# Optimization experiments

Measured on AMD Instinct MI355X. Metric: run time of the kernel, lower is better.

## Reference

```python
import jax, jax.numpy as jnp
import numpy as np

STRIDES = (2, 2, 2)  # from init_kwargs


def _sparse_conv3d_transpose(images, kernel, default_value, base_plane, strides):
    """Sparse masked 3D transposed conv driven by a per-pixel depth base plane.

    images:     [B, Hi, Wi, Di, C]  stored slab of active voxels per pixel
    kernel:     [kH, kW, kD, F, C]
    base_plane: [B, Ho, Wo, 1] int  starting VIRTUAL depth of the output slab
    Output virtual depth of voxel (ho, wo, do) is base_plane[ho, wo] + do.
    Input slab start (in input-depth units) at input pixel (hi, wi) is
    base_plane[hi*sH, wi*sW] // sD. SAME-style padding ((k-1)//2).
    Out-of-slab / out-of-bounds taps read default_value (frozen zero).
    """
    B, Hi, Wi, Di, C = images.shape
    k0, k1, k2, F, _ = kernel.shape
    s0, s1, s2 = strides
    bp = base_plane[..., 0]                       # [B, Ho, Wo]
    Ho, Wo = bp.shape[1], bp.shape[2]
    Do = Di * s2
    p0, p1, p2 = (k0 - 1) // 2, (k1 - 1) // 2, (k2 - 1) // 2
    bp_in = bp[:, ::s0, ::s1] // s2               # [B, Hi, Wi] input slab start
    b_idx = jnp.arange(B)[:, None, None]
    vd = bp[..., None] + jnp.arange(Do)           # [B, Ho, Wo, Do] virtual out depth
    ho = jnp.arange(Ho)
    wo = jnp.arange(Wo)
    out = jnp.zeros((B, Ho, Wo, Do, F), images.dtype)
    for kh in range(k0):
        hn = ho + p0 - kh
        hok = (hn % s0 == 0) & (hn >= 0) & (hn < Hi * s0)
        hi = jnp.clip(hn // s0, 0, Hi - 1)
        for kw in range(k1):
            wn = wo + p1 - kw
            wok = (wn % s1 == 0) & (wn >= 0) & (wn < Wi * s1)
            wi = jnp.clip(wn // s1, 0, Wi - 1)
            sp_ok = hok[None, :, None] & wok[None, None, :]              # [1,Ho,Wo]
            bpg = bp_in[b_idx, hi[None, :, None], wi[None, None, :]]     # [B,Ho,Wo]
            for kd in range(k2):
                dn = vd + p2 - kd                                        # [B,Ho,Wo,Do]
                dok = (dn % s2) == 0
                di = dn // s2 - bpg[..., None]
                mask = sp_ok[..., None] & dok & (di >= 0) & (di < Di)
                dic = jnp.clip(di, 0, Di - 1)
                # gather [B,Ho,Wo,Do,C]
                vals = images[b_idx[..., None], hi[None, :, None, None],
                              wi[None, None, :, None], dic]
                vals = jnp.where(mask[..., None], vals, default_value)
                out = out + jnp.einsum('bhwdc,fc->bhwdf', vals, kernel[kh, kw, kd])
    return out


def setup_inputs() -> dict:
    key = jax.random.key(0)
    k1, k2, k3 = jax.random.split(key, 3)
    B, Hi, Wi, Di, C, F = 2, 64, 64, 32, 16, 8
    images = jax.random.normal(k1, (B, Hi, Wi, Di, C), dtype=jnp.float32)
    base_plane = jax.random.randint(k2, (B, Hi * 2, Wi * 2, 1), 0, 16, dtype=jnp.int32)
    kernel = jax.random.normal(k3, (3, 3, 3, F, C), dtype=jnp.float32) * 0.1
    default_value = jnp.zeros((), dtype=jnp.float32)  # frozen, zeros initializer
    return {"images": images, "base_plane": base_plane,
            "kernel": kernel, "default_value": default_value}


def reference(images, base_plane, kernel, default_value):
    return _sparse_conv3d_transpose(images, kernel, default_value, base_plane, STRIDES)
```

## Files before the change

kernel.cpp:

```cpp
#include <hip/hip_runtime.h>

constexpr int Bc  = 2;
constexpr int HiC = 64, WiC = 64, DiC = 32;
constexpr int Cc  = 16, Fc  = 8;
constexpr int HoC = 128, WoC = 128, DoC = 64;

constexpr int SLAB_SHORTS = DiC * Cc;
constexpr int NSLAB       = 18;
constexpr int ZOFF        = NSLAB * SLAB_SHORTS * 2;

typedef __attribute__((ext_vector_type(8))) short short8;
typedef __attribute__((ext_vector_type(4))) float f32x4;

__device__ alignas(16) const float FZERO[8] = {0, 0, 0, 0, 0, 0, 0, 0};

__device__ __forceinline__ unsigned pk2(float x, float y) {
    unsigned ux = __float_as_uint(x), uy = __float_as_uint(y);
    ux += ((ux >> 16) & 1u) + 0x7FFFu;
    uy += ((uy >> 16) & 1u) + 0x7FFFu;
    return (ux >> 16) | (uy & 0xFFFF0000u);
}
__device__ __forceinline__ short8 pack8(float4 a, float4 b) {
    union { unsigned u[4]; short8 s; } r;
    r.u[0] = pk2(a.x, a.y); r.u[1] = pk2(a.z, a.w);
    r.u[2] = pk2(b.x, b.y); r.u[3] = pk2(b.z, b.w);
    return r.s;
}

template<int CLS>
__device__ __forceinline__ void doCols(const short* __restrict__ slabs,
                                       const int*   __restrict__ bp,
                                       const float* __restrict__ kern,
                                       float*       __restrict__ out,
                                       float*       __restrict__ ldsw,
                                       int b, int ho, int wo0, int wi0, int lane) {
    constexpr int NP = (CLS == 0) ? 1 : ((CLS == 3) ? 4 : 2);
    constexpr int OP = (NP + 1) / 2;
    constexpr int KH[4][4] = {{1,0,0,0},{1,1,0,0},{0,2,0,0},{0,0,2,2}};
    constexpr int KW[4][4] = {{1,0,0,0},{0,2,0,0},{1,1,0,0},{0,2,0,2}};

    const int quad = lane >> 4, n = lane & 15;
    const int half = quad >> 1, chalf = quad & 1;
    const int chalfB = chalf * 16;

    short8 bE[NP], bO[OP];
    #pragma unroll
    for (int p = 0; p < NP; ++p) {
        const int kp = KH[CLS][p] * 3 + KW[CLS][p];
        const float* wp = (n < Fc)
            ? kern + (kp * 3 + 2 * half) * 128 + n * 16 + chalf * 8 : FZERO;
        bE[p] = pack8(*(const float4*)wp, *(const float4*)(wp + 4));
    }
    #pragma unroll
    for (int pp = 0; pp < OP; ++pp) {
        const int  PA   = (2 * pp < NP) ? 2 * pp : 0;
        const bool hasB = (2 * pp + 1) < NP;
        const int  PB   = hasB ? (2 * pp + 1) : 0;
        const int kpa = KH[CLS][PA] * 3 + KW[CLS][PA];
        const int kpb = KH[CLS][PB] * 3 + KW[CLS][PB];
        const int kp  = half ? kpb : kpa;
        const bool v  = (n < Fc) && (!half || hasB);
        const float* wp = v ? kern + (kp * 3 + 1) * 128 + n * 16 + chalf * 8 : FZERO;
        bO[pp] = pack8(*(const float4*)wp, *(const float4*)(wp + 4));
    }

    int colx[4], bpcol[4], bpgr[4][NP], pxo[4][NP]; bool pvs[4][NP];
    #pragma unroll
    for (int cc = 0; cc < 4; ++cc) {
        const int wo = wo0 + 2 * cc;
        colx[cc]  = __builtin_amdgcn_readfirstlane((b * HoC + ho) * WoC + wo);
        bpcol[cc] = bp[colx[cc]];
        #pragma unroll
        for (int p = 0; p < NP; ++p) {
            const int kh = KH[CLS][p], kw = KW[CLS][p];
            int hi = (ho + 1 - kh) >> 1; hi = hi > HiC - 1 ? HiC - 1 : hi;
            int wi = (wo + 1 - kw) >> 1; wi = wi > WiC - 1 ? WiC - 1 : wi;
            pvs[cc][p] = (kh != 0 || ho + 1 < HoC) && (kw != 0 || wo + 1 < WoC);
            const int sidx =
                __builtin_amdgcn_readfirstlane((b * HoC + 2 * hi) * WoC + 2 * wi);
            bpgr[cc][p] = bp[sidx];
            const int hidx = (kh == 0) ? 1 : 0;
            pxo[cc][p] = __builtin_amdgcn_readfirstlane(
                             (hidx * 9 + (wi - wi0)) << 10);
        }
    }

    #pragma unroll
    for (int cc = 0; cc < 4; ++cc) {
        const int bp_col = bpcol[cc];
        const int q      = (bp_col + 1) & 1;
        const int baseE  = (bp_col + q + 1) >> 1;
        const int baseO  = (bp_col + 1 - q) >> 1;
        int sE[NP], sO[NP];
        #pragma unroll
        for (int p = 0; p < NP; ++p) {
            const int bpg = bpgr[cc][p] >> 1;
            sE[p] = pvs[cc][p] ? baseE - bpg : -100000;
            sO[p] = pvs[cc][p] ? baseO - bpg : -100000;
        }

        f32x4 accE[2] = {{0.f,0.f,0.f,0.f},{0.f,0.f,0.f,0.f}};
        f32x4 accO[2] = {{0.f,0.f,0.f,0.f},{0.f,0.f,0.f,0.f}};

        #pragma unroll
        for (int g = 0; g < 2; ++g) {
            #pragma unroll
            for (int p = 0; p < NP; ++p) {
                const int  di = sE[p] + 16 * g + n - half;
                const bool ok = (unsigned)di < (unsigned)DiC;
                const int  off = ok ? pxo[cc][p] + di * 32 + chalfB : ZOFF;
                short8 a = *(const short8*)((const char*)slabs + off);
                accE[g] = __builtin_amdgcn_mfma_f32_16x16x32_bf16(a, bE[p], accE[g], 0, 0, 0);
            }
            #pragma unroll
            for (int pp = 0; pp < OP; ++pp) {
                const int  PA   = (2 * pp < NP) ? 2 * pp : 0;
                const bool hasB = (2 * pp + 1) < NP;
                const int  PB   = hasB ? (2 * pp + 1) : 0;
                const int  sOs  = half ? (hasB ? sO[PB] : -100000) : sO[PA];
                const int  pxs  = half ? pxo[cc][PB] : pxo[cc][PA];
                const int  di = sOs + 16 * g + n;
                const bool ok = (unsigned)di < (unsigned)DiC;
                const int  off = ok ? pxs + di * 32 + chalfB : ZOFF;
                short8 a = *(const short8*)((const char*)slabs + off);
                accO[g] = __builtin_amdgcn_mfma_f32_16x16x32_bf16(a, bO[pp], accO[g], 0, 0, 0);
            }
        }

        __builtin_amdgcn_wave_barrier();
        if (n < Fc) {
            #pragma unroll
            for (int g = 0; g < 2; ++g) {
                #pragma unroll
                for (int r = 0; r < 4; ++r) {
                    const int m2 = 16 * g + quad * 4 + r;
                    ldsw[(2 * m2 + q) * Fc + n]     = accE[g][r];
                    ldsw[(2 * m2 + 1 - q) * Fc + n] = accO[g][r];
                }
            }
        }
        __builtin_amdgcn_wave_barrier();
        float* outc = out + (size_t)colx[cc] * (DoC * Fc);
        *(float4*)(outc + lane * 8)     = *(const float4*)(ldsw + lane * 8);
        *(float4*)(outc + lane * 8 + 4) = *(const float4*)(ldsw + lane * 8 + 4);
        __builtin_amdgcn_wave_barrier();
    }
}

__global__ __launch_bounds__(256, 4)
void sconv_mfma(const float* __restrict__ img, const int* __restrict__ bp,
                const float* __restrict__ kern, float* __restrict__ out) {
    __shared__ short slabs[NSLAB * SLAB_SHORTS + 8];
    __shared__ float lds[4 * DoC * Fc];
    const int t = threadIdx.x, wv = t >> 6, lane = t & 63;
    const int b = blockIdx.z, r = blockIdx.y;
    const int wo0 = (blockIdx.x << 4) + (wv & 1) + ((wv >> 1) << 3);
    const int wi0 = blockIdx.x << 3;
    float* ldsw = lds + wv * (DoC * Fc);

    const int hi0 = r;
    int hi1 = r + 1; if (hi1 > HiC - 1) hi1 = HiC - 1;
    #pragma unroll
    for (int k = 0; k < 5; ++k) {
        const int s = wv + 4 * k;
        if (s < NSLAB) {
            const int hi = (s >= 9) ? hi1 : hi0;
            int wi = wi0 + ((s >= 9) ? s - 9 : s); if (wi > WiC - 1) wi = WiC - 1;
            const float* g = img + (((b * HiC + hi) * WiC + wi) << 9) + lane * 8;
            float4 v0 = *(const float4*)g;
            float4 v1 = *(const float4*)(g + 4);
            *(short8*)&slabs[(s << 9) + lane * 8] = pack8(v0, v1);
        }
    }
    if (t < 8) slabs[NSLAB * SLAB_SHORTS + t] = 0;
    __syncthreads();

    if (wv & 1) {
        doCols<1>(slabs, bp, kern, out, ldsw, b, 2 * r,     wo0, wi0, lane);
        doCols<3>(slabs, bp, kern, out, ldsw, b, 2 * r + 1, wo0, wi0, lane);
    } else {
        doCols<0>(slabs, bp, kern, out, ldsw, b, 2 * r,     wo0, wi0, lane);
        doCols<2>(slabs, bp, kern, out, ldsw, b, 2 * r + 1, wo0, wi0, lane);
    }
}

extern "C" void kernel_launch(void* const* d_in, const int* in_sizes, int n_in,
                              void* d_out, int out_size, void* d_ws, size_t ws_size,
                              hipStream_t stream) {
    const float* images = (const float*)d_in[0];
    const int*   bp     = (const int*)d_in[1];
    const float* kern   = (const float*)d_in[2];
    float* out = (float*)d_out;
    (void)d_ws; (void)ws_size;

    dim3 grid(WoC / 16, HoC / 2, Bc), block(256);
    hipLaunchKernelGGL(sconv_mfma, grid, block, 0, stream,
                       images, bp, kern, out);
}
```

Baseline: 94.54 us.

## Stage bf16 kernel weights in LDS and de-template the column loops

Converts the whole filter to bf16 once per block and keeps it in shared memory, so each wave no longer reads and packs weights from global memory. The templated, fully unrolled per-class code is replaced by a single runtime-parameterised body with non-unrolled loops and bit-packed kh/kw tables. The aim is a smaller binary with lower register pressure. In exchange it gives up instruction-level parallelism across taps and columns, and adds runtime index arithmetic, serialized boundary-plane loads and extra LDS traffic per block.

```diff
diff --git a/kernel.cpp b/kernel.cpp
--- a/kernel.cpp
+++ b/kernel.cpp
@@ -5,14 +5,13 @@
 constexpr int Cc  = 16, Fc  = 8;
 constexpr int HoC = 128, WoC = 128, DoC = 64;
 
-constexpr int SLAB_SHORTS = DiC * Cc;
-constexpr int NSLAB       = 18;
-constexpr int ZOFF        = NSLAB * SLAB_SHORTS * 2;
+constexpr int NSLAB = 18;
+constexpr int ZOFFB = NSLAB * 1024;
+constexpr int KBUFB = ZOFFB + 16;
+constexpr int SL_SHORTS = (KBUFB + 27 * 256) / 2;
 
 typedef __attribute__((ext_vector_type(8))) short short8;
 typedef __attribute__((ext_vector_type(4))) float f32x4;
-
-__device__ alignas(16) const float FZERO[8] = {0, 0, 0, 0, 0, 0, 0, 0};
 
 __device__ __forceinline__ unsigned pk2(float x, float y) {
     unsigned ux = __float_as_uint(x), uy = __float_as_uint(y);
@@ -27,120 +26,113 @@
     return r.s;
 }
 
-template<int CLS>
-__device__ __forceinline__ void doCols(const short* __restrict__ slabs,
-                                       const int*   __restrict__ bp,
-                                       const float* __restrict__ kern,
-                                       float*       __restrict__ out,
-                                       float*       __restrict__ ldsw,
-                                       int b, int ho, int wo0, int wi0, int lane) {
-    constexpr int NP = (CLS == 0) ? 1 : ((CLS == 3) ? 4 : 2);
-    constexpr int OP = (NP + 1) / 2;
-    constexpr int KH[4][4] = {{1,0,0,0},{1,1,0,0},{0,2,0,0},{0,0,2,2}};
-    constexpr int KW[4][4] = {{1,0,0,0},{0,2,0,0},{1,1,0,0},{0,2,0,2}};
-
+__device__ __forceinline__ void colsBody(const short* __restrict__ sl,
+                                         const int*   __restrict__ bp,
+                                         float*       __restrict__ out,
+                                         float*       __restrict__ ldsw,
+                                         int b, int ho, int wo0, int wi0,
+                                         int lane, int cls) {
+    const unsigned KHP = 0xA0080501u, KWP = 0x88050801u;
+    const int np = (cls == 0) ? 1 : ((cls == 3) ? 4 : 2);
+    const int op = (np + 1) >> 1;
+    const int shb = cls * 8;
     const int quad = lane >> 4, n = lane & 15;
     const int half = quad >> 1, chalf = quad & 1;
     const int chalfB = chalf * 16;
 
-    short8 bE[NP], bO[OP];
-    #pragma unroll
-    for (int p = 0; p < NP; ++p) {
-        const int kp = KH[CLS][p] * 3 + KW[CLS][p];
-        const float* wp = (n < Fc)
-            ? kern + (kp * 3 + 2 * half) * 128 + n * 16 + chalf * 8 : FZERO;
-        bE[p] = pack8(*(const float4*)wp, *(const float4*)(wp + 4));
-    }
-    #pragma unroll
-    for (int pp = 0; pp < OP; ++pp) {
-        const int  PA   = (2 * pp < NP) ? 2 * pp : 0;
-        const bool hasB = (2 * pp + 1) < NP;
-        const int  PB   = hasB ? (2 * pp + 1) : 0;
-        const int kpa = KH[CLS][PA] * 3 + KW[CLS][PA];
-        const int kpb = KH[CLS][PB] * 3 + KW[CLS][PB];
-        const int kp  = half ? kpb : kpa;
-        const bool v  = (n < Fc) && (!half || hasB);
-        const float* wp = v ? kern + (kp * 3 + 1) * 128 + n * 16 + chalf * 8 : FZERO;
-        bO[pp] = pack8(*(const float4*)wp, *(const float4*)(wp + 4));
-    }
-
-    int colx[4], bpcol[4], bpgr[4][NP], pxo[4][NP]; bool pvs[4][NP];
-    #pragma unroll
+    #pragma unroll 1
     for (int cc = 0; cc < 4; ++cc) {
-        const int wo = wo0 + 2 * cc;
-        colx[cc]  = __builtin_amdgcn_readfirstlane((b * HoC + ho) * WoC + wo);
-        bpcol[cc] = bp[colx[cc]];
-        #pragma unroll
-        for (int p = 0; p < NP; ++p) {
-            const int kh = KH[CLS][p], kw = KW[CLS][p];
-            int hi = (ho + 1 - kh) >> 1; hi = hi > HiC - 1 ? HiC - 1 : hi;
-            int wi = (wo + 1 - kw) >> 1; wi = wi > WiC - 1 ? WiC - 1 : wi;
-            pvs[cc][p] = (kh != 0 || ho + 1 < HoC) && (kw != 0 || wo + 1 < WoC);
-            const int sidx =
-                __builtin_amdgcn_readfirstlane((b * HoC + 2 * hi) * WoC + 2 * wi);
-            bpgr[cc][p] = bp[sidx];
-            const int hidx = (kh == 0) ? 1 : 0;
-            pxo[cc][p] = __builtin_amdgcn_readfirstlane(
-                             (hidx * 9 + (wi - wi0)) << 10);
-        }
-    }
-
-    #pragma unroll
-    for (int cc = 0; cc < 4; ++cc) {
-        const int bp_col = bpcol[cc];
+        const int wo   = wo0 + 2 * cc;
+        const int colx = __builtin_amdgcn_readfirstlane((b * HoC + ho) * WoC + wo);
+        const int bp_col = bp[colx];
         const int q      = (bp_col + 1) & 1;
         const int baseE  = (bp_col + q + 1) >> 1;
         const int baseO  = (bp_col + 1 - q) >> 1;
-        int sE[NP], sO[NP];
-        #pragma unroll
-        for (int p = 0; p < NP; ++p) {
-            const int bpg = bpgr[cc][p] >> 1;
-            sE[p] = pvs[cc][p] ? baseE - bpg : -100000;
-            sO[p] = pvs[cc][p] ? baseO - bpg : -100000;
+
+        f32x4 accE0{0.f,0.f,0.f,0.f}, accE1{0.f,0.f,0.f,0.f};
+        f32x4 accO0{0.f,0.f,0.f,0.f}, accO1{0.f,0.f,0.f,0.f};
+
+        #pragma unroll 1
+        for (int p = 0; p < np; ++p) {
+            const int kh = (KHP >> (shb + 2 * p)) & 3;
+            const int kw = (KWP >> (shb + 2 * p)) & 3;
+            int hi = (ho + 1 - kh) >> 1; hi = hi > HiC - 1 ? HiC - 1 : hi;
+            int wi = (wo + 1 - kw) >> 1; wi = wi > WiC - 1 ? WiC - 1 : wi;
+            const bool pvs = (kh != 0 || ho + 1 < HoC) && (kw != 0 || wo + 1 < WoC);
+            const int bpg = bp[__builtin_amdgcn_readfirstlane(
+                                   (b * HoC + 2 * hi) * WoC + 2 * wi)];
+            const int pxo = __builtin_amdgcn_readfirstlane(
+                                (((kh == 0) ? 1 : 0) * 9 + (wi - wi0)) << 10);
+            const int sE  = pvs ? baseE - (bpg >> 1) : -100000;
+            const int kp  = kh * 3 + kw;
+            const int bofs = (n < Fc)
+                ? (KBUFB + (kp * 3 + 2 * half) * 256 + n * 32 + chalfB) : ZOFFB;
+            short8 bf = *(const short8*)((const char*)sl + bofs);
+
+            int di  = sE + n - half;
+            int off = ((unsigned)di < (unsigned)DiC) ? pxo + di * 32 + chalfB : ZOFFB;
+            short8 a = *(const short8*)((const char*)sl + off);
+            accE0 = __builtin_amdgcn_mfma_f32_16x16x32_bf16(a, bf, accE0, 0, 0, 0);
+            di += 16;
+            off = ((unsigned)di < (unsigned)DiC) ? pxo + di * 32 + chalfB : ZOFFB;
+            a = *(const short8*)((const char*)sl + off);
+            accE1 = __builtin_amdgcn_mfma_f32_16x16x32_bf16(a, bf, accE1, 0, 0, 0);
         }
 
-        f32x4 accE[2] = {{0.f,0.f,0.f,0.f},{0.f,0.f,0.f,0.f}};
-        f32x4 accO[2] = {{0.f,0.f,0.f,0.f},{0.f,0.f,0.f,0.f}};
+        #pragma unroll 1
+        for (int pp = 0; pp < op; ++pp) {
+            const int  pA   = 2 * pp;
+            const bool hasB = (2 * pp + 1) < np;
+            const int  pB   = hasB ? 2 * pp + 1 : pA;
+            const int khA = (KHP >> (shb + 2 * pA)) & 3, kwA = (KWP >> (shb + 2 * pA)) & 3;
+            const int khB = (KHP >> (shb + 2 * pB)) & 3, kwB = (KWP >> (shb + 2 * pB)) & 3;
+            int hiA = (ho + 1 - khA) >> 1; hiA = hiA > HiC - 1 ? HiC - 1 : hiA;
+            int wiA = (wo + 1 - kwA) >> 1; wiA = wiA > WiC - 1 ? WiC - 1 : wiA;
+            int hiB = (ho + 1 - khB) >> 1; hiB = hiB > HiC - 1 ? HiC - 1 : hiB;
+            int wiB = (wo + 1 - kwB) >> 1; wiB = wiB > WiC - 1 ? WiC - 1 : wiB;
+            const bool pvsA = (khA != 0 || ho + 1 < HoC) && (kwA != 0 || wo + 1 < WoC);
+            const bool pvsB = (khB != 0 || ho + 1 < HoC) && (kwB != 0 || wo + 1 < WoC);
+            const int bpgA = bp[__builtin_amdgcn_readfirstlane(
+                                    (b * HoC + 2 * hiA) * WoC + 2 * wiA)];
+            const int bpgB = bp[__builtin_amdgcn_readfirstlane(
+                                    (b * HoC + 2 * hiB) * WoC + 2 * wiB)];
+            const int pxoA = __builtin_amdgcn_readfirstlane(
+                                 (((khA == 0) ? 1 : 0) * 9 + (wiA - wi0)) << 10);
+            const int pxoB = __builtin_amdgcn_readfirstlane(
+                                 (((khB == 0) ? 1 : 0) * 9 + (wiB - wi0)) << 10);
+            const int sOA = pvsA ? baseO - (bpgA >> 1) : -100000;
+            const int sOB = (hasB && pvsB) ? baseO - (bpgB >> 1) : -100000;
+            const int sOs = half ? sOB : sOA;
+            const int pxs = half ? pxoB : pxoA;
+            const int kps = half ? khB * 3 + kwB : khA * 3 + kwA;
+            const int bofs = (n < Fc && (!half || hasB))
+                ? (KBUFB + (kps * 3 + 1) * 256 + n * 32 + chalfB) : ZOFFB;
+            short8 bf = *(const short8*)((const char*)sl + bofs);
 
-        #pragma unroll
-        for (int g = 0; g < 2; ++g) {
-            #pragma unroll
-            for (int p = 0; p < NP; ++p) {
-                const int  di = sE[p] + 16 * g + n - half;
-                const bool ok = (unsigned)di < (unsigned)DiC;
-                const int  off = ok ? pxo[cc][p] + di * 32 + chalfB : ZOFF;
-                short8 a = *(const short8*)((const char*)slabs + off);
-                accE[g] = __builtin_amdgcn_mfma_f32_16x16x32_bf16(a, bE[p], accE[g], 0, 0, 0);
-            }
-            #pragma unroll
-            for (int pp = 0; pp < OP; ++pp) {
-                const int  PA   = (2 * pp < NP) ? 2 * pp : 0;
-                const bool hasB = (2 * pp + 1) < NP;
-                const int  PB   = hasB ? (2 * pp + 1) : 0;
-                const int  sOs  = half ? (hasB ? sO[PB] : -100000) : sO[PA];
-                const int  pxs  = half ? pxo[cc][PB] : pxo[cc][PA];
-                const int  di = sOs + 16 * g + n;
-                const bool ok = (unsigned)di < (unsigned)DiC;
-                const int  off = ok ? pxs + di * 32 + chalfB : ZOFF;
-                short8 a = *(const short8*)((const char*)slabs + off);
-                accO[g] = __builtin_amdgcn_mfma_f32_16x16x32_bf16(a, bO[pp], accO[g], 0, 0, 0);
-            }
+            int di  = sOs + n;
+            int off = ((unsigned)di < (unsigned)DiC) ? pxs + di * 32 + chalfB : ZOFFB;
+            short8 a = *(const short8*)((const char*)sl + off);
+            accO0 = __builtin_amdgcn_mfma_f32_16x16x32_bf16(a, bf, accO0, 0, 0, 0);
+            di += 16;
+            off = ((unsigned)di < (unsigned)DiC) ? pxs + di * 32 + chalfB : ZOFFB;
+            a = *(const short8*)((const char*)sl + off);
+            accO1 = __builtin_amdgcn_mfma_f32_16x16x32_bf16(a, bf, accO1, 0, 0, 0);
         }
 
         __builtin_amdgcn_wave_barrier();
         if (n < Fc) {
             #pragma unroll
-            for (int g = 0; g < 2; ++g) {
-                #pragma unroll
-                for (int r = 0; r < 4; ++r) {
-                    const int m2 = 16 * g + quad * 4 + r;
-                    ldsw[(2 * m2 + q) * Fc + n]     = accE[g][r];
-                    ldsw[(2 * m2 + 1 - q) * Fc + n] = accO[g][r];
-                }
+            for (int rr = 0; rr < 4; ++rr) {
+                int m2 = quad * 4 + rr;
+                ldsw[(2 * m2 + q) * Fc + n]     = accE0[rr];
+                ldsw[(2 * m2 + 1 - q) * Fc + n] = accO0[rr];
+                m2 += 16;
+                ldsw[(2 * m2 + q) * Fc + n]     = accE1[rr];
+                ldsw[(2 * m2 + 1 - q) * Fc + n] = accO1[rr];
             }
         }
         __builtin_amdgcn_wave_barrier();
-        float* outc = out + (size_t)colx[cc] * (DoC * Fc);
+        float* outc = out + (size_t)colx * (DoC * Fc);
         *(float4*)(outc + lane * 8)     = *(const float4*)(ldsw + lane * 8);
         *(float4*)(outc + lane * 8 + 4) = *(const float4*)(ldsw + lane * 8 + 4);
         __builtin_amdgcn_wave_barrier();
@@ -150,38 +142,34 @@
 __global__ __launch_bounds__(256, 4)
 void sconv_mfma(const float* __restrict__ img, const int* __restrict__ bp,
                 const float* __restrict__ kern, float* __restrict__ out) {
-    __shared__ short slabs[NSLAB * SLAB_SHORTS + 8];
-    __shared__ float lds[4 * DoC * Fc];
+    __shared__ alignas(16) short sl[SL_SHORTS];
+    __shared__ float ldsT[4 * DoC * Fc];
     const int t = threadIdx.x, wv = t >> 6, lane = t & 63;
     const int b = blockIdx.z, r = blockIdx.y;
     const int wo0 = (blockIdx.x << 4) + (wv & 1) + ((wv >> 1) << 3);
     const int wi0 = blockIdx.x << 3;
-    float* ldsw = lds + wv * (DoC * Fc);
+    float* ldsw = ldsT + wv * (DoC * Fc);
 
     const int hi0 = r;
     int hi1 = r + 1; if (hi1 > HiC - 1) hi1 = HiC - 1;
-    #pragma unroll
-    for (int k = 0; k < 5; ++k) {
-        const int s = wv + 4 * k;
-        if (s < NSLAB) {
-            const int hi = (s >= 9) ? hi1 : hi0;
-            int wi = wi0 + ((s >= 9) ? s - 9 : s); if (wi > WiC - 1) wi = WiC - 1;
-            const float* g = img + (((b * HiC + hi) * WiC + wi) << 9) + lane * 8;
-            float4 v0 = *(const float4*)g;
-            float4 v1 = *(const float4*)(g + 4);
-            *(short8*)&slabs[(s << 9) + lane * 8] = pack8(v0, v1);
-        }
+    #pragma unroll 1
+    for (int s = wv; s < NSLAB; s += 4) {
+        const int hi = (s >= 9) ? hi1 : hi0;
+        int wi = wi0 + ((s >= 9) ? s - 9 : s); if (wi > WiC - 1) wi = WiC - 1;
+        const float* g = img + (((b * HiC + hi) * WiC + wi) << 9) + lane * 8;
+        *(short8*)&sl[(s << 9) + lane * 8] =
+            pack8(*(const float4*)g, *(const float4*)(g + 4));
     }
-    if (t < 8) slabs[NSLAB * SLAB_SHORTS + t] = 0;
+    #pragma unroll 1
+    for (int i = t; i < 1728; i += 256)
+        ((unsigned*)((char*)sl + KBUFB))[i] = pk2(kern[2 * i], kern[2 * i + 1]);
+    if (t < 8) sl[ZOFFB / 2 + t] = 0;
     __syncthreads();
 
-    if (wv & 1) {
-        doCols<1>(slabs, bp, kern, out, ldsw, b, 2 * r,     wo0, wi0, lane);
-        doCols<3>(slabs, bp, kern, out, ldsw, b, 2 * r + 1, wo0, wi0, lane);
-    } else {
-        doCols<0>(slabs, bp, kern, out, ldsw, b, 2 * r,     wo0, wi0, lane);
-        doCols<2>(slabs, bp, kern, out, ldsw, b, 2 * r + 1, wo0, wi0, lane);
-    }
+    const int p = wv & 1;
+    #pragma unroll 1
+    for (int hs = 0; hs < 2; ++hs)
+        colsBody(sl, bp, out, ldsw, b, 2 * r + hs, wo0, wi0, lane, 2 * hs + p);
 }
 
 extern "C" void kernel_launch(void* const* d_in, const int* in_sizes, int n_in,
```

Result: slower. 99.99 us (+5.8%).
